# Optimization experiments

Measured on AMD Instinct MI355X. Metric: run time of the kernel, lower is better.

## Reference

```python
import jax, jax.numpy as jnp
import numpy as np

N = 100_000      # nodes
E = 3_200_000    # edges (avg degree 32)
H = 16           # hidden channels
C_IN, C_OUT = 1, 2


def setup_inputs() -> dict:
    key = jax.random.key(0)
    k1, k2, k3, k4, k5 = jax.random.split(key, 5)
    x = jax.random.normal(k1, (N, C_IN), dtype=jnp.float32)
    src = jax.random.randint(k2, (E,), 0, N, dtype=jnp.int32)
    dst = jax.random.randint(k3, (E,), 0, N, dtype=jnp.int32)
    edge_index = jnp.stack([src, dst])  # [2, E], PyG layout
    # Glorot-style init for the two linear transforms
    W1 = jax.random.normal(k4, (C_IN, H), dtype=jnp.float32) * np.sqrt(2.0 / (C_IN + H))
    b1 = jnp.zeros((H,), dtype=jnp.float32)
    W2 = jax.random.normal(k5, (H, C_OUT), dtype=jnp.float32) * np.sqrt(2.0 / (H + C_OUT))
    b2 = jnp.zeros((C_OUT,), dtype=jnp.float32)
    return {"x": x, "edge_index": edge_index, "W1": W1, "b1": b1, "W2": W2, "b2": b2}


def _gcn_conv(x, src, dst, W, b):
    """GCNConv: out = D^{-1/2} (A+I) D^{-1/2} X W + b.
    src/dst already include self-loops. x: [N, Cin], W: [Cin, Cout]."""
    deg = jax.ops.segment_sum(jnp.ones_like(dst, dtype=x.dtype), dst, num_segments=N)
    dinv = jnp.where(deg > 0, jax.lax.rsqrt(jnp.maximum(deg, 1.0)), 0.0)
    norm = dinv[src] * dinv[dst]                       # [E+N]
    h = x @ W                                          # transform first (Cin small)
    msg = norm[:, None] * h[src]                       # [E+N, Cout]
    out = jax.ops.segment_sum(msg, dst, num_segments=N)
    return out + b


def reference(x, edge_index, W1, b1, W2, b2):
    loops = jnp.arange(N, dtype=edge_index.dtype)
    src = jnp.concatenate([edge_index[0], loops])      # add self-loops
    dst = jnp.concatenate([edge_index[1], loops])
    h = _gcn_conv(x, src, dst, W1, b1)
    h = jax.nn.relu(h)
    out = _gcn_conv(h, src, dst, W2, b2)
    return out
```

## Files before the change

kernel.cpp:

```cpp
#include <hip/hip_runtime.h>

#define NN 100000
#define NE 3200000
#define HC 16

#define BKT_BITS 7
#define BKT_NODES 128
#define NB 782
#define NB1 783
#define CHUNK_S 8192
#define NCH 391
#define NCCP 392
#define MCAP 5120
#define PADW (((unsigned)NN << BKT_BITS) | (BKT_NODES - 1))

typedef unsigned uv4 __attribute__((ext_vector_type(4)));
typedef int      iv4 __attribute__((ext_vector_type(4)));


__global__ __launch_bounds__(512) void k_sortchunk(const int* __restrict__ src,
                                                   const int* __restrict__ dst,
                                                   unsigned short* __restrict__ Hoff,
                                                   unsigned* __restrict__ binned) {
    __shared__ unsigned h[NB1];
    __shared__ unsigned sorted[CHUNK_S];
    __shared__ unsigned wsum[8];
    int tid = threadIdx.x;
    int c = blockIdx.x;
    int b0 = c * CHUNK_S;
    int e1 = min(b0 + CHUNK_S, NE);
    int cnt = e1 - b0;

    for (int j = tid; j < NB1; j += 512) h[j] = 0;
    __syncthreads();

    iv4 dreg[4], sreg[4];
    int nit = 0;
    for (int v = b0 + tid * 4; v + 3 < e1; v += 2048) {
        iv4 d4 = *(const iv4*)(dst + v);
        iv4 s4 = *(const iv4*)(src + v);
        dreg[nit] = d4; sreg[nit] = s4; ++nit;
        atomicAdd(&h[((unsigned)d4.x) >> BKT_BITS], 1u);
        atomicAdd(&h[((unsigned)d4.y) >> BKT_BITS], 1u);
        atomicAdd(&h[((unsigned)d4.z) >> BKT_BITS], 1u);
        atomicAdd(&h[((unsigned)d4.w) >> BKT_BITS], 1u);
    }
    __syncthreads();

    int i0 = tid * 2;
    unsigned v0 = (i0 + 0 < NB1) ? h[i0 + 0] : 0;
    unsigned v1 = (i0 + 1 < NB1) ? h[i0 + 1] : 0;
    unsigned lsum = v0 + v1;
    unsigned sc = lsum;
#pragma unroll
    for (int off = 1; off < 64; off <<= 1) {
        unsigned u = __shfl_up(sc, off, 64);
        if ((tid & 63) >= off) sc += u;
    }
    int wave = tid >> 6;
    if ((tid & 63) == 63) wsum[wave] = sc;
    __syncthreads();
    unsigned wpre = 0;
    for (int w = 0; w < wave; ++w) wpre += wsum[w];
    unsigned excl = wpre + sc - lsum;
    __syncthreads();
    if (i0 + 0 < NB1) h[i0 + 0] = excl;
    if (i0 + 1 < NB1) h[i0 + 1] = excl + v0;

    unsigned short* row = Hoff + (size_t)c * NB1;
    if (i0 + 0 < NB1) row[i0 + 0] = (unsigned short)excl;
    if (i0 + 1 < NB1) row[i0 + 1] = (unsigned short)(excl + v0);
    __syncthreads();

    int it = 0;
    for (int v = b0 + tid * 4; v + 3 < e1; v += 2048, ++it) {
        iv4 d4 = dreg[it];
        iv4 s4 = sreg[it];
        {   unsigned d = (unsigned)d4.x, s = (unsigned)s4.x;
            unsigned pos = atomicAdd(&h[d >> BKT_BITS], 1u);
            sorted[pos] = (s << BKT_BITS) | (d & (BKT_NODES - 1)); }
        {   unsigned d = (unsigned)d4.y, s = (unsigned)s4.y;
            unsigned pos = atomicAdd(&h[d >> BKT_BITS], 1u);
            sorted[pos] = (s << BKT_BITS) | (d & (BKT_NODES - 1)); }
        {   unsigned d = (unsigned)d4.z, s = (unsigned)s4.z;
            unsigned pos = atomicAdd(&h[d >> BKT_BITS], 1u);
            sorted[pos] = (s << BKT_BITS) | (d & (BKT_NODES - 1)); }
        {   unsigned d = (unsigned)d4.w, s = (unsigned)s4.w;
            unsigned pos = atomicAdd(&h[d >> BKT_BITS], 1u);
            sorted[pos] = (s << BKT_BITS) | (d & (BKT_NODES - 1)); }
    }
    __syncthreads();

    unsigned* out = binned + (size_t)c * CHUNK_S;
    for (int j = tid * 4; j + 3 < cnt; j += 2048)
        *(uv4*)(out + j) = *(const uv4*)(sorted + j);
}


__global__ __launch_bounds__(256) void k_transT(const unsigned short* __restrict__ Hoff,
                                                unsigned short* __restrict__ TH) {
    __shared__ unsigned short tile[32][33];
    int tx = threadIdx.x & 31;
    int ty0 = (threadIdx.x >> 5) * 4;
    int c0 = blockIdx.x * 32;
    int b0 = blockIdx.y * 32;
#pragma unroll
    for (int k = 0; k < 4; ++k) {
        int c = c0 + ty0 + k, b = b0 + tx;
        tile[ty0 + k][tx] = (c < NCH && b < NB1) ? Hoff[(size_t)c * NB1 + b] : (unsigned short)0;
    }
    __syncthreads();
#pragma unroll
    for (int k = 0; k < 4; ++k) {
        int b = b0 + ty0 + k, c = c0 + tx;
        if (b < NB1 && c < NCH) TH[(size_t)b * NCCP + c] = tile[tx][ty0 + k];
    }
}


__global__ __launch_bounds__(64) void k_totals(const unsigned short* __restrict__ TH,
                                               unsigned* __restrict__ totals) {
    int b = blockIdx.x;
    int lane = threadIdx.x;
    const unsigned short* r0 = TH + (size_t)b * NCCP;
    const unsigned short* r1 = r0 + NCCP;
    unsigned s = 0;
    for (int c = lane; c < NCH; c += 64) s += (unsigned)r1[c] - (unsigned)r0[c];
#pragma unroll
    for (int off = 32; off >= 1; off >>= 1) s += __shfl_xor(s, off, 64);
    if (lane == 0) totals[b] = s;
}

__global__ __launch_bounds__(1024) void k_base2(const unsigned* __restrict__ totals,
                                                unsigned* __restrict__ gbase) {
    __shared__ unsigned s[1024];
    int t = threadIdx.x;
    unsigned v = (t < NB) ? ((totals[t] + 15u) & ~15u) : 0;
    s[t] = v;
    __syncthreads();
    for (int off = 1; off < 1024; off <<= 1) {
        unsigned u = (t >= off) ? s[t - off] : 0;
        __syncthreads();
        s[t] += u;
        __syncthreads();
    }
    if (t < NB) gbase[t] = s[t] - v;
}


__global__ __launch_bounds__(256) void k_merge_deg(const unsigned* __restrict__ binned,
                                                   const unsigned short* __restrict__ TH,
                                                   const unsigned* __restrict__ gbase,
                                                   const float* __restrict__ x,
                                                   unsigned* __restrict__ merged,
                                                   unsigned short* __restrict__ cofsg,
                                                   float* __restrict__ dinv,
                                                   float* __restrict__ p) {
    __shared__ unsigned short th0s[NCH];
    __shared__ unsigned short lens[NCH];
    __shared__ unsigned S[NCH + 1];
    __shared__ unsigned wsum[4];
    __shared__ unsigned cnt[BKT_NODES];
    __shared__ unsigned stage[MCAP];
    __shared__ unsigned short cof[BKT_NODES + 2];
    __shared__ unsigned wsA;
    int tid = threadIdx.x, b = blockIdx.x;

    const unsigned short* r0 = TH + (size_t)b * NCCP;
    const unsigned short* r1 = r0 + NCCP;
    for (int c = tid; c < NCH; c += 256) {
        unsigned a = r0[c];
        th0s[c] = (unsigned short)a;
        lens[c] = (unsigned short)((unsigned)r1[c] - a);
    }
    if (tid < BKT_NODES) cnt[tid] = 0;
    __syncthreads();

    int i0 = tid * 2;
    unsigned v0 = (i0 + 0 < NCH) ? (unsigned)lens[i0 + 0] : 0;
    unsigned v1 = (i0 + 1 < NCH) ? (unsigned)lens[i0 + 1] : 0;
    unsigned lsum = v0 + v1;
    unsigned sc = lsum;
#pragma unroll
    for (int off = 1; off < 64; off <<= 1) {
        unsigned u = __shfl_up(sc, off, 64);
        if ((tid & 63) >= off) sc += u;
    }
    int wave = tid >> 6;
    if ((tid & 63) == 63) wsum[wave] = sc;
    __syncthreads();
    unsigned wpre = 0;
    for (int w = 0; w < wave; ++w) wpre += wsum[w];
    unsigned excl = wpre + sc - lsum;
    if (i0 + 0 <= NCH) S[i0 + 0] = excl;
    if (i0 + 1 <= NCH) S[i0 + 1] = excl + v0;
    __syncthreads();

    unsigned T = S[NCH];
    unsigned Tr = (T + 15u) & ~15u;
    unsigned gb = gbase[b];
    if (tid < 16) {
        unsigned q = T + tid;
        if (q < Tr) stage[q] = PADW;
    }

    for (int c = tid; c < NCH; c += 256) {
        unsigned off = th0s[c], L = lens[c];
        if (!L) continue;
        unsigned base = S[c];
        const unsigned* segbase = binned + (size_t)c * CHUNK_S;
        unsigned je = off + L;
        for (unsigned j4 = off & ~3u; j4 < je; j4 += 4) {
            uv4 e4 = *(const uv4*)(segbase + j4);
#pragma unroll
            for (int k = 0; k < 4; ++k) {
                unsigned j = j4 + (unsigned)k;
                if (j >= off && j < je) {
                    unsigned e = ((const unsigned*)&e4)[k];
                    atomicAdd(&cnt[e & (BKT_NODES - 1)], 1u);
                    stage[base + (j - off)] = e;
                }
            }
        }
    }
    __syncthreads();

    for (unsigned j = tid * 4; j < Tr; j += 1024)
        *(uv4*)(merged + gb + j) = *(const uv4*)(stage + j);

    unsigned cv = (tid < BKT_NODES) ? cnt[tid] : 0u;
    unsigned csc = cv;
#pragma unroll
    for (int off = 1; off < 64; off <<= 1) {
        unsigned u = __shfl_up(csc, off, 64);
        if ((tid & 63) >= off) csc += u;
    }
    if (tid == 63) wsA = csc;
    __syncthreads();
    if (tid < BKT_NODES) {
        unsigned incl = csc + ((tid >= 64) ? wsA : 0u);
        cof[tid + 1] = (unsigned short)incl;
    }
    if (tid == 0) cof[0] = 0;
    __syncthreads();
    if (tid < BKT_NODES + 1)
        cofsg[(size_t)b * (BKT_NODES + 2) + tid] = cof[tid];

    int node = b * BKT_NODES + tid;
    if (tid < BKT_NODES) {
        if (node < NN) {
            float di = rsqrtf((float)(cnt[tid] + 1u));
            dinv[node] = di;
            p[node] = di * x[node];
        } else if (node == NN) {
            p[node] = 0.f;
        }
    }
}


__global__ __launch_bounds__(512) void k_agg1(unsigned* __restrict__ merged,
                                              const unsigned* __restrict__ gbase,
                                              const unsigned* __restrict__ totals,
                                              const unsigned short* __restrict__ cofsg,
                                              const float* __restrict__ dinv,
                                              const float* __restrict__ p,
                                              const float* __restrict__ W1,
                                              const float* __restrict__ b1,
                                              const float* __restrict__ W2,
                                              float2* __restrict__ g) {
    __shared__ unsigned short cof[BKT_NODES + 2];
    __shared__ unsigned cur[BKT_NODES + 1];
    __shared__ unsigned se[MCAP];
    __shared__ float part[512];
    int tid = threadIdx.x, b = blockIdx.x;
    if (tid < BKT_NODES + 1) cof[tid] = cofsg[(size_t)b * (BKT_NODES + 2) + tid];
    __syncthreads();
    if (tid < BKT_NODES + 1) cur[tid] = cof[tid];
    __syncthreads();
    unsigned Tr = (totals[b] + 15u) & ~15u;
    unsigned* m = merged + gbase[b];
    for (unsigned j = tid * 4; j < Tr; j += 2048) {
        uv4 e = *(const uv4*)(m + j);
        { unsigned w = e.x; unsigned sl = (w >> BKT_BITS >= NN) ? 128u : (w & (BKT_NODES - 1));
          se[atomicAdd(&cur[sl], 1u)] = w >> BKT_BITS; }
        { unsigned w = e.y; unsigned sl = (w >> BKT_BITS >= NN) ? 128u : (w & (BKT_NODES - 1));
          se[atomicAdd(&cur[sl], 1u)] = w >> BKT_BITS; }
        { unsigned w = e.z; unsigned sl = (w >> BKT_BITS >= NN) ? 128u : (w & (BKT_NODES - 1));
          se[atomicAdd(&cur[sl], 1u)] = w >> BKT_BITS; }
        { unsigned w = e.w; unsigned sl = (w >> BKT_BITS >= NN) ? 128u : (w & (BKT_NODES - 1));
          se[atomicAdd(&cur[sl], 1u)] = w >> BKT_BITS; }
    }
    __syncthreads();

    for (unsigned j = tid * 4; j < Tr; j += 2048)
        *(uv4*)(m + j) = *(const uv4*)(se + j);

    int nl = tid >> 2, q = tid & 3;
    unsigned o0 = cof[nl], o1 = cof[nl + 1];
    unsigned len = o1 - o0;
    unsigned s = o0 + ((len * q) >> 2);
    unsigned e = o0 + ((len * (q + 1)) >> 2);
    float sum = 0.f;
    unsigned i = s;
    for (; i + 3 < e; i += 4) {
        unsigned a0 = se[i], a1 = se[i + 1], a2 = se[i + 2], a3 = se[i + 3];
        float x0 = p[a0], x1 = p[a1], x2 = p[a2], x3 = p[a3];
        sum += (x0 + x1) + (x2 + x3);
    }
    for (; i < e; ++i) sum += p[se[i]];
    part[tid] = sum;
    __syncthreads();

    if (q == 0) {
        int node = b * BKT_NODES + nl;
        if (node < NN) {
            float di = dinv[node];
            float sf = di * (part[tid] + part[tid + 1] + part[tid + 2] + part[tid + 3]
                             + p[node]);
            float g0 = 0.f, g1 = 0.f;
#pragma unroll
            for (int c = 0; c < HC; ++c) {
                float h = fmaxf(fmaf(sf, W1[c], b1[c]), 0.f);
                g0 = fmaf(h, W2[2 * c], g0);
                g1 = fmaf(h, W2[2 * c + 1], g1);
            }
            g[node] = make_float2(di * g0, di * g1);
        }
    }
}


__global__ __launch_bounds__(512) void k_agg2(const unsigned* __restrict__ merged,
                                              const unsigned* __restrict__ gbase,
                                              const unsigned* __restrict__ totals,
                                              const unsigned short* __restrict__ cofsg,
                                              const float* __restrict__ dinv,
                                              const float2* __restrict__ g,
                                              const float* __restrict__ b2,
                                              float2* __restrict__ out) {
    __shared__ unsigned short cof[BKT_NODES + 2];
    __shared__ unsigned se[MCAP];
    __shared__ float2 part[512];
    int tid = threadIdx.x, b = blockIdx.x;
    if (tid < BKT_NODES + 1) cof[tid] = cofsg[(size_t)b * (BKT_NODES + 2) + tid];
    unsigned Tr = (totals[b] + 15u) & ~15u;
    const unsigned* m = merged + gbase[b];
    for (unsigned j = tid * 4; j < Tr; j += 2048)
        *(uv4*)(se + j) = *(const uv4*)(m + j);
    __syncthreads();

    int nl = tid >> 2, q = tid & 3;
    unsigned o0 = cof[nl], o1 = cof[nl + 1];
    unsigned len = o1 - o0;
    unsigned s = o0 + ((len * q) >> 2);
    unsigned e = o0 + ((len * (q + 1)) >> 2);
    float sx = 0.f, sy = 0.f;
    unsigned i = s;
    for (; i + 3 < e; i += 4) {
        unsigned a0 = se[i], a1 = se[i + 1], a2 = se[i + 2], a3 = se[i + 3];
        float2 v0 = g[a0], v1 = g[a1], v2 = g[a2], v3 = g[a3];
        sx += (v0.x + v1.x) + (v2.x + v3.x);
        sy += (v0.y + v1.y) + (v2.y + v3.y);
    }
    for (; i < e; ++i) { float2 v = g[se[i]]; sx += v.x; sy += v.y; }
    part[tid] = make_float2(sx, sy);
    __syncthreads();

    if (q == 0) {
        int node = b * BKT_NODES + nl;
        if (node < NN) {
            float di = dinv[node];
            float2 me = g[node];
            float ax = part[tid].x + part[tid + 1].x + part[tid + 2].x + part[tid + 3].x + me.x;
            float ay = part[tid].y + part[tid + 1].y + part[tid + 2].y + part[tid + 3].y + me.y;
            out[node] = make_float2(fmaf(di, ax, b2[0]), fmaf(di, ay, b2[1]));
        }
    }
}


__global__ __launch_bounds__(256) void f_deg(const int* __restrict__ dst,
                                             unsigned int* __restrict__ deg, int E) {
    int i = blockIdx.x * blockDim.x + threadIdx.x;
    if (i < E) atomicAdd(&deg[dst[i]], 1u);
}
__global__ __launch_bounds__(256) void f_node1(const float* __restrict__ x,
                                               const unsigned int* __restrict__ deg,
                                               float* __restrict__ dinv, float* __restrict__ p,
                                               float* __restrict__ t, int N) {
    int i = blockIdx.x * blockDim.x + threadIdx.x;
    if (i < N) {
        float di = rsqrtf((float)(deg[i] + 1u));
        dinv[i] = di; float pi = di * x[i]; p[i] = pi; t[i] = pi;
    }
}
__global__ __launch_bounds__(256) void f_scatter1(const int* __restrict__ src,
                                                  const int* __restrict__ dst,
                                                  const float* __restrict__ p,
                                                  float* __restrict__ t, int E) {
    int i = blockIdx.x * blockDim.x + threadIdx.x;
    if (i < E) atomicAdd(&t[dst[i]], p[src[i]]);
}
__global__ __launch_bounds__(256) void f_node2(const float* __restrict__ dinv,
                                               const float* __restrict__ t,
                                               const float* __restrict__ W1,
                                               const float* __restrict__ b1,
                                               const float* __restrict__ W2,
                                               float2* __restrict__ g,
                                               float2* __restrict__ acc, int N) {
    int i = blockIdx.x * blockDim.x + threadIdx.x;
    if (i < N) {
        float di = dinv[i]; float s = di * t[i];
        float g0 = 0.f, g1 = 0.f;
#pragma unroll
        for (int c = 0; c < HC; ++c) {
            float h = fmaxf(fmaf(s, W1[c], b1[c]), 0.f);
            g0 = fmaf(h, W2[2 * c], g0); g1 = fmaf(h, W2[2 * c + 1], g1);
        }
        float2 gv = make_float2(di * g0, di * g1);
        g[i] = gv; acc[i] = gv;
    }
}
__global__ __launch_bounds__(256) void f_scatter2(const int* __restrict__ src,
                                                  const int* __restrict__ dst,
                                                  const float2* __restrict__ g,
                                                  float* __restrict__ acc, int E) {
    int i = blockIdx.x * blockDim.x + threadIdx.x;
    if (i < E) {
        int s = src[i], d = dst[i];
        float2 gv = g[s];
        atomicAdd(&acc[2 * d], gv.x);
        atomicAdd(&acc[2 * d + 1], gv.y);
    }
}
__global__ __launch_bounds__(256) void f_out(const float* __restrict__ dinv,
                                             const float* __restrict__ b2,
                                             float* __restrict__ out, int N) {
    int i = blockIdx.x * blockDim.x + threadIdx.x;
    if (i < N) {
        float di = dinv[i];
        out[2 * i]     = fmaf(di, out[2 * i],     b2[0]);
        out[2 * i + 1] = fmaf(di, out[2 * i + 1], b2[1]);
    }
}

extern "C" void kernel_launch(void* const* d_in, const int* in_sizes, int n_in,
                              void* d_out, int out_size, void* d_ws, size_t ws_size,
                              hipStream_t stream) {
    const float* x  = (const float*)d_in[0];
    const int* ei   = (const int*)d_in[1];
    const int* src  = ei;
    const int* dst  = ei + NE;
    const float* W1 = (const float*)d_in[2];
    const float* b1 = (const float*)d_in[3];
    const float* W2 = (const float*)d_in[4];
    const float* b2 = (const float*)d_in[5];

    const int BT = 256;
    const int gridE = (NE + BT - 1) / BT;
    const int gridN = (NN + BT - 1) / BT;

    size_t need = 0;
    auto carve = [&](size_t bytes) { size_t o = need; need += (bytes + 255) & ~(size_t)255; return o; };
    size_t o_Hoff = carve((size_t)NCH * NB1 * 2);
    size_t o_TH   = carve((size_t)NB1 * NCCP * 2);
    size_t o_tot  = carve((size_t)NB * 4);
    size_t o_gb   = carve((size_t)(NB + 1) * 4);
    size_t o_cofs = carve((size_t)NB * (BKT_NODES + 2) * 2);
    size_t o_dinv = carve((size_t)NN * 4);
    size_t o_p    = carve((size_t)(NN + 1) * 4);
    size_t o_g    = carve((size_t)(NN + 1) * 8);
    size_t o_bin  = carve((size_t)NCH * CHUNK_S * 4);
    size_t o_mrg  = carve((size_t)(NE + 16 * NB + 64) * 4);

    if (ws_size >= need) {
        char* ws = (char*)d_ws;
        unsigned short* Hoff = (unsigned short*)(ws + o_Hoff);
        unsigned short* TH   = (unsigned short*)(ws + o_TH);
        unsigned* totals = (unsigned*)(ws + o_tot);
        unsigned* gbase  = (unsigned*)(ws + o_gb);
        unsigned short* cofs = (unsigned short*)(ws + o_cofs);
        float*    dinv   = (float*)(ws + o_dinv);
        float*    p      = (float*)(ws + o_p);
        float2*   g      = (float2*)(ws + o_g);
        unsigned* binned = (unsigned*)(ws + o_bin);
        unsigned* merged = (unsigned*)(ws + o_mrg);

        k_sortchunk<<<NCH, 512, 0, stream>>>(src, dst, Hoff, binned);
        k_transT   <<<dim3(13, 25), 256, 0, stream>>>(Hoff, TH);
        k_totals   <<<NB, 64, 0, stream>>>(TH, totals);
        k_base2    <<<1, 1024, 0, stream>>>(totals, gbase);
        k_merge_deg<<<NB, 256, 0, stream>>>(binned, TH, gbase, x, merged, cofs, dinv, p);
        k_agg1     <<<NB, 512, 0, stream>>>(merged, gbase, totals, cofs, dinv, p, W1, b1, W2, g);
        k_agg2     <<<NB, 512, 0, stream>>>(merged, gbase, totals, cofs, dinv, g, b2, (float2*)d_out);
    } else {
        float* out = (float*)d_out;
        char* ws = (char*)d_ws;
        unsigned int* deg = (unsigned int*)ws;
        float* dinv = (float*)(ws + 1 * sizeof(float) * NN);
        float* p    = (float*)(ws + 2 * sizeof(float) * NN);
        float* t    = (float*)(ws + 3 * sizeof(float) * NN);
        float2* g   = (float2*)(ws + 4 * sizeof(float) * NN);

        hipMemsetAsync(deg, 0, NN * sizeof(unsigned int), stream);
        f_deg<<<gridE, BT, 0, stream>>>(dst, deg, NE);
        f_node1<<<gridN, BT, 0, stream>>>(x, deg, dinv, p, t, NN);
        f_scatter1<<<gridE, BT, 0, stream>>>(src, dst, p, t, NE);
        f_node2<<<gridN, BT, 0, stream>>>(dinv, t, W1, b1, W2, g, (float2*)out, NN);
        f_scatter2<<<gridE, BT, 0, stream>>>(src, dst, g, out, NE);
        f_out<<<gridN, BT, 0, stream>>>(dinv, b2, out, NN);
    }
}
```

Before: 148.8 us.

## Replace chunk sort/merge pipeline with atomic-reserved fixed-capacity bucket regions

```diff
diff --git a/kernel.cpp b/kernel.cpp
--- a/kernel.cpp
+++ b/kernel.cpp
@@ -7,31 +7,25 @@
 #define BKT_BITS 7
 #define BKT_NODES 128
 #define NB 782
-#define NB1 783
 #define CHUNK_S 8192
 #define NCH 391
-#define NCCP 392
 #define MCAP 5120
-#define PADW (((unsigned)NN << BKT_BITS) | (BKT_NODES - 1))
 
 typedef unsigned uv4 __attribute__((ext_vector_type(4)));
 typedef int      iv4 __attribute__((ext_vector_type(4)));
 
 
-__global__ __launch_bounds__(512) void k_sortchunk(const int* __restrict__ src,
-                                                   const int* __restrict__ dst,
-                                                   unsigned short* __restrict__ Hoff,
-                                                   unsigned* __restrict__ binned) {
-    __shared__ unsigned h[NB1];
-    __shared__ unsigned sorted[CHUNK_S];
-    __shared__ unsigned wsum[8];
+__global__ __launch_bounds__(512) void k_bin(const int* __restrict__ src,
+                                             const int* __restrict__ dst,
+                                             unsigned* __restrict__ gcur,
+                                             unsigned* __restrict__ regions) {
+    __shared__ unsigned h[NB];
     int tid = threadIdx.x;
     int c = blockIdx.x;
     int b0 = c * CHUNK_S;
     int e1 = min(b0 + CHUNK_S, NE);
-    int cnt = e1 - b0;
-
-    for (int j = tid; j < NB1; j += 512) h[j] = 0;
+
+    for (int j = tid; j < NB; j += 512) h[j] = 0;
     __syncthreads();
 
     iv4 dreg[4], sreg[4];
@@ -47,29 +41,10 @@
     }
     __syncthreads();
 
-    int i0 = tid * 2;
-    unsigned v0 = (i0 + 0 < NB1) ? h[i0 + 0] : 0;
-    unsigned v1 = (i0 + 1 < NB1) ? h[i0 + 1] : 0;
-    unsigned lsum = v0 + v1;
-    unsigned sc = lsum;
-#pragma unroll
-    for (int off = 1; off < 64; off <<= 1) {
-        unsigned u = __shfl_up(sc, off, 64);
-        if ((tid & 63) >= off) sc += u;
-    }
-    int wave = tid >> 6;
-    if ((tid & 63) == 63) wsum[wave] = sc;
-    __syncthreads();
-    unsigned wpre = 0;
-    for (int w = 0; w < wave; ++w) wpre += wsum[w];
-    unsigned excl = wpre + sc - lsum;
-    __syncthreads();
-    if (i0 + 0 < NB1) h[i0 + 0] = excl;
-    if (i0 + 1 < NB1) h[i0 + 1] = excl + v0;
-
-    unsigned short* row = Hoff + (size_t)c * NB1;
-    if (i0 + 0 < NB1) row[i0 + 0] = (unsigned short)excl;
-    if (i0 + 1 < NB1) row[i0 + 1] = (unsigned short)(excl + v0);
+    for (int j = tid; j < NB; j += 512) {
+        unsigned cEdges = h[j];
+        if (cEdges) h[j] = (unsigned)j * MCAP + atomicAdd(&gcur[j], cEdges);
+    }
     __syncthreads();
 
     int it = 0;
@@ -78,246 +53,93 @@
         iv4 s4 = sreg[it];
         {   unsigned d = (unsigned)d4.x, s = (unsigned)s4.x;
             unsigned pos = atomicAdd(&h[d >> BKT_BITS], 1u);
-            sorted[pos] = (s << BKT_BITS) | (d & (BKT_NODES - 1)); }
+            regions[pos] = (s << BKT_BITS) | (d & (BKT_NODES - 1)); }
         {   unsigned d = (unsigned)d4.y, s = (unsigned)s4.y;
             unsigned pos = atomicAdd(&h[d >> BKT_BITS], 1u);
-            sorted[pos] = (s << BKT_BITS) | (d & (BKT_NODES - 1)); }
+            regions[pos] = (s << BKT_BITS) | (d & (BKT_NODES - 1)); }
         {   unsigned d = (unsigned)d4.z, s = (unsigned)s4.z;
             unsigned pos = atomicAdd(&h[d >> BKT_BITS], 1u);
-            sorted[pos] = (s << BKT_BITS) | (d & (BKT_NODES - 1)); }
+            regions[pos] = (s << BKT_BITS) | (d & (BKT_NODES - 1)); }
         {   unsigned d = (unsigned)d4.w, s = (unsigned)s4.w;
             unsigned pos = atomicAdd(&h[d >> BKT_BITS], 1u);
-            sorted[pos] = (s << BKT_BITS) | (d & (BKT_NODES - 1)); }
-    }
-    __syncthreads();
-
-    unsigned* out = binned + (size_t)c * CHUNK_S;
-    for (int j = tid * 4; j + 3 < cnt; j += 2048)
-        *(uv4*)(out + j) = *(const uv4*)(sorted + j);
-}
-
-
-__global__ __launch_bounds__(256) void k_transT(const unsigned short* __restrict__ Hoff,
-                                                unsigned short* __restrict__ TH) {
-    __shared__ unsigned short tile[32][33];
-    int tx = threadIdx.x & 31;
-    int ty0 = (threadIdx.x >> 5) * 4;
-    int c0 = blockIdx.x * 32;
-    int b0 = blockIdx.y * 32;
-#pragma unroll
-    for (int k = 0; k < 4; ++k) {
-        int c = c0 + ty0 + k, b = b0 + tx;
-        tile[ty0 + k][tx] = (c < NCH && b < NB1) ? Hoff[(size_t)c * NB1 + b] : (unsigned short)0;
-    }
-    __syncthreads();
-#pragma unroll
-    for (int k = 0; k < 4; ++k) {
-        int b = b0 + ty0 + k, c = c0 + tx;
-        if (b < NB1 && c < NCH) TH[(size_t)b * NCCP + c] = tile[tx][ty0 + k];
-    }
-}
-
-
-__global__ __launch_bounds__(64) void k_totals(const unsigned short* __restrict__ TH,
-                                               unsigned* __restrict__ totals) {
-    int b = blockIdx.x;
-    int lane = threadIdx.x;
-    const unsigned short* r0 = TH + (size_t)b * NCCP;
-    const unsigned short* r1 = r0 + NCCP;
-    unsigned s = 0;
-    for (int c = lane; c < NCH; c += 64) s += (unsigned)r1[c] - (unsigned)r0[c];
-#pragma unroll
-    for (int off = 32; off >= 1; off >>= 1) s += __shfl_xor(s, off, 64);
-    if (lane == 0) totals[b] = s;
-}
-
-__global__ __launch_bounds__(1024) void k_base2(const unsigned* __restrict__ totals,
-                                                unsigned* __restrict__ gbase) {
-    __shared__ unsigned s[1024];
-    int t = threadIdx.x;
-    unsigned v = (t < NB) ? ((totals[t] + 15u) & ~15u) : 0;
-    s[t] = v;
-    __syncthreads();
-    for (int off = 1; off < 1024; off <<= 1) {
-        unsigned u = (t >= off) ? s[t - off] : 0;
-        __syncthreads();
-        s[t] += u;
-        __syncthreads();
-    }
-    if (t < NB) gbase[t] = s[t] - v;
-}
-
-
-__global__ __launch_bounds__(256) void k_merge_deg(const unsigned* __restrict__ binned,
-                                                   const unsigned short* __restrict__ TH,
-                                                   const unsigned* __restrict__ gbase,
-                                                   const float* __restrict__ x,
-                                                   unsigned* __restrict__ merged,
-                                                   unsigned short* __restrict__ cofsg,
-                                                   float* __restrict__ dinv,
-                                                   float* __restrict__ p) {
-    __shared__ unsigned short th0s[NCH];
-    __shared__ unsigned short lens[NCH];
-    __shared__ unsigned S[NCH + 1];
-    __shared__ unsigned wsum[4];
+            regions[pos] = (s << BKT_BITS) | (d & (BKT_NODES - 1)); }
+    }
+}
+
+
+__global__ __launch_bounds__(256) void k_deg(const unsigned* __restrict__ regions,
+                                             const unsigned* __restrict__ gcur,
+                                             const float* __restrict__ x,
+                                             float* __restrict__ dinv,
+                                             float* __restrict__ p) {
     __shared__ unsigned cnt[BKT_NODES];
-    __shared__ unsigned stage[MCAP];
-    __shared__ unsigned short cof[BKT_NODES + 2];
-    __shared__ unsigned wsA;
     int tid = threadIdx.x, b = blockIdx.x;
-
-    const unsigned short* r0 = TH + (size_t)b * NCCP;
-    const unsigned short* r1 = r0 + NCCP;
-    for (int c = tid; c < NCH; c += 256) {
-        unsigned a = r0[c];
-        th0s[c] = (unsigned short)a;
-        lens[c] = (unsigned short)((unsigned)r1[c] - a);
-    }
     if (tid < BKT_NODES) cnt[tid] = 0;
     __syncthreads();
 
-    int i0 = tid * 2;
-    unsigned v0 = (i0 + 0 < NCH) ? (unsigned)lens[i0 + 0] : 0;
-    unsigned v1 = (i0 + 1 < NCH) ? (unsigned)lens[i0 + 1] : 0;
-    unsigned lsum = v0 + v1;
-    unsigned sc = lsum;
-#pragma unroll
-    for (int off = 1; off < 64; off <<= 1) {
-        unsigned u = __shfl_up(sc, off, 64);
-        if ((tid & 63) >= off) sc += u;
-    }
-    int wave = tid >> 6;
-    if ((tid & 63) == 63) wsum[wave] = sc;
-    __syncthreads();
-    unsigned wpre = 0;
-    for (int w = 0; w < wave; ++w) wpre += wsum[w];
-    unsigned excl = wpre + sc - lsum;
-    if (i0 + 0 <= NCH) S[i0 + 0] = excl;
-    if (i0 + 1 <= NCH) S[i0 + 1] = excl + v0;
-    __syncthreads();
-
-    unsigned T = S[NCH];
-    unsigned Tr = (T + 15u) & ~15u;
-    unsigned gb = gbase[b];
-    if (tid < 16) {
-        unsigned q = T + tid;
-        if (q < Tr) stage[q] = PADW;
-    }
-
-    for (int c = tid; c < NCH; c += 256) {
-        unsigned off = th0s[c], L = lens[c];
-        if (!L) continue;
-        unsigned base = S[c];
-        const unsigned* segbase = binned + (size_t)c * CHUNK_S;
-        unsigned je = off + L;
-        for (unsigned j4 = off & ~3u; j4 < je; j4 += 4) {
-            uv4 e4 = *(const uv4*)(segbase + j4);
-#pragma unroll
-            for (int k = 0; k < 4; ++k) {
-                unsigned j = j4 + (unsigned)k;
-                if (j >= off && j < je) {
-                    unsigned e = ((const unsigned*)&e4)[k];
-                    atomicAdd(&cnt[e & (BKT_NODES - 1)], 1u);
-                    stage[base + (j - off)] = e;
-                }
-            }
-        }
-    }
-    __syncthreads();
-
-    for (unsigned j = tid * 4; j < Tr; j += 1024)
-        *(uv4*)(merged + gb + j) = *(const uv4*)(stage + j);
-
-    unsigned cv = (tid < BKT_NODES) ? cnt[tid] : 0u;
-    unsigned csc = cv;
-#pragma unroll
-    for (int off = 1; off < 64; off <<= 1) {
-        unsigned u = __shfl_up(csc, off, 64);
-        if ((tid & 63) >= off) csc += u;
-    }
-    if (tid == 63) wsA = csc;
-    __syncthreads();
+    unsigned sz = gcur[b];
+    const unsigned* r = regions + (size_t)b * MCAP;
+    unsigned sz4 = sz & ~3u;
+    for (unsigned j = (unsigned)tid * 4; j < sz4; j += 1024) {
+        uv4 e = *(const uv4*)(r + j);
+        atomicAdd(&cnt[e.x & (BKT_NODES - 1)], 1u);
+        atomicAdd(&cnt[e.y & (BKT_NODES - 1)], 1u);
+        atomicAdd(&cnt[e.z & (BKT_NODES - 1)], 1u);
+        atomicAdd(&cnt[e.w & (BKT_NODES - 1)], 1u);
+    }
+    for (unsigned j = sz4 + (unsigned)tid; j < sz; j += 256)
+        atomicAdd(&cnt[r[j] & (BKT_NODES - 1)], 1u);
+    __syncthreads();
+
     if (tid < BKT_NODES) {
-        unsigned incl = csc + ((tid >= 64) ? wsA : 0u);
-        cof[tid + 1] = (unsigned short)incl;
-    }
-    if (tid == 0) cof[0] = 0;
-    __syncthreads();
-    if (tid < BKT_NODES + 1)
-        cofsg[(size_t)b * (BKT_NODES + 2) + tid] = cof[tid];
-
-    int node = b * BKT_NODES + tid;
-    if (tid < BKT_NODES) {
+        int node = b * BKT_NODES + tid;
         if (node < NN) {
             float di = rsqrtf((float)(cnt[tid] + 1u));
             dinv[node] = di;
             p[node] = di * x[node];
-        } else if (node == NN) {
-            p[node] = 0.f;
         }
     }
 }
 
 
-__global__ __launch_bounds__(512) void k_agg1(unsigned* __restrict__ merged,
-                                              const unsigned* __restrict__ gbase,
-                                              const unsigned* __restrict__ totals,
-                                              const unsigned short* __restrict__ cofsg,
+__global__ __launch_bounds__(256) void k_agg1(const unsigned* __restrict__ regions,
+                                              const unsigned* __restrict__ gcur,
                                               const float* __restrict__ dinv,
                                               const float* __restrict__ p,
                                               const float* __restrict__ W1,
                                               const float* __restrict__ b1,
                                               const float* __restrict__ W2,
                                               float2* __restrict__ g) {
-    __shared__ unsigned short cof[BKT_NODES + 2];
-    __shared__ unsigned cur[BKT_NODES + 1];
-    __shared__ unsigned se[MCAP];
-    __shared__ float part[512];
+    __shared__ float acc[BKT_NODES];
     int tid = threadIdx.x, b = blockIdx.x;
-    if (tid < BKT_NODES + 1) cof[tid] = cofsg[(size_t)b * (BKT_NODES + 2) + tid];
-    __syncthreads();
-    if (tid < BKT_NODES + 1) cur[tid] = cof[tid];
-    __syncthreads();
-    unsigned Tr = (totals[b] + 15u) & ~15u;
-    unsigned* m = merged + gbase[b];
-    for (unsigned j = tid * 4; j < Tr; j += 2048) {
-        uv4 e = *(const uv4*)(m + j);
-        { unsigned w = e.x; unsigned sl = (w >> BKT_BITS >= NN) ? 128u : (w & (BKT_NODES - 1));
-          se[atomicAdd(&cur[sl], 1u)] = w >> BKT_BITS; }
-        { unsigned w = e.y; unsigned sl = (w >> BKT_BITS >= NN) ? 128u : (w & (BKT_NODES - 1));
-          se[atomicAdd(&cur[sl], 1u)] = w >> BKT_BITS; }
-        { unsigned w = e.z; unsigned sl = (w >> BKT_BITS >= NN) ? 128u : (w & (BKT_NODES - 1));
-          se[atomicAdd(&cur[sl], 1u)] = w >> BKT_BITS; }
-        { unsigned w = e.w; unsigned sl = (w >> BKT_BITS >= NN) ? 128u : (w & (BKT_NODES - 1));
-          se[atomicAdd(&cur[sl], 1u)] = w >> BKT_BITS; }
-    }
-    __syncthreads();
-
-    for (unsigned j = tid * 4; j < Tr; j += 2048)
-        *(uv4*)(m + j) = *(const uv4*)(se + j);
-
-    int nl = tid >> 2, q = tid & 3;
-    unsigned o0 = cof[nl], o1 = cof[nl + 1];
-    unsigned len = o1 - o0;
-    unsigned s = o0 + ((len * q) >> 2);
-    unsigned e = o0 + ((len * (q + 1)) >> 2);
-    float sum = 0.f;
-    unsigned i = s;
-    for (; i + 3 < e; i += 4) {
-        unsigned a0 = se[i], a1 = se[i + 1], a2 = se[i + 2], a3 = se[i + 3];
-        float x0 = p[a0], x1 = p[a1], x2 = p[a2], x3 = p[a3];
-        sum += (x0 + x1) + (x2 + x3);
-    }
-    for (; i < e; ++i) sum += p[se[i]];
-    part[tid] = sum;
-    __syncthreads();
-
-    if (q == 0) {
-        int node = b * BKT_NODES + nl;
+    if (tid < BKT_NODES) acc[tid] = 0.f;
+    __syncthreads();
+
+    unsigned sz = gcur[b];
+    const unsigned* r = regions + (size_t)b * MCAP;
+    unsigned sz4 = sz & ~3u;
+    for (unsigned j = (unsigned)tid * 4; j < sz4; j += 1024) {
+        uv4 e = *(const uv4*)(r + j);
+        float p0 = p[e.x >> BKT_BITS];
+        float p1 = p[e.y >> BKT_BITS];
+        float p2 = p[e.z >> BKT_BITS];
+        float p3 = p[e.w >> BKT_BITS];
+        atomicAdd(&acc[e.x & (BKT_NODES - 1)], p0);
+        atomicAdd(&acc[e.y & (BKT_NODES - 1)], p1);
+        atomicAdd(&acc[e.z & (BKT_NODES - 1)], p2);
+        atomicAdd(&acc[e.w & (BKT_NODES - 1)], p3);
+    }
+    for (unsigned j = sz4 + (unsigned)tid; j < sz; j += 256) {
+        unsigned e = r[j];
+        atomicAdd(&acc[e & (BKT_NODES - 1)], p[e >> BKT_BITS]);
+    }
+    __syncthreads();
+
+    if (tid < BKT_NODES) {
+        int node = b * BKT_NODES + tid;
         if (node < NN) {
             float di = dinv[node];
-            float sf = di * (part[tid] + part[tid + 1] + part[tid + 2] + part[tid + 3]
-                             + p[node]);
+            float sf = di * (acc[tid] + p[node]);
             float g0 = 0.f, g1 = 0.f;
 #pragma unroll
             for (int c = 0; c < HC; ++c) {
@@ -331,49 +153,51 @@
 }
 
 
-__global__ __launch_bounds__(512) void k_agg2(const unsigned* __restrict__ merged,
-                                              const unsigned* __restrict__ gbase,
-                                              const unsigned* __restrict__ totals,
-                                              const unsigned short* __restrict__ cofsg,
+__global__ __launch_bounds__(256) void k_agg2(const unsigned* __restrict__ regions,
+                                              const unsigned* __restrict__ gcur,
                                               const float* __restrict__ dinv,
                                               const float2* __restrict__ g,
                                               const float* __restrict__ b2,
                                               float2* __restrict__ out) {
-    __shared__ unsigned short cof[BKT_NODES + 2];
-    __shared__ unsigned se[MCAP];
-    __shared__ float2 part[512];
+    __shared__ float accx[BKT_NODES];
+    __shared__ float accy[BKT_NODES];
     int tid = threadIdx.x, b = blockIdx.x;
-    if (tid < BKT_NODES + 1) cof[tid] = cofsg[(size_t)b * (BKT_NODES + 2) + tid];
-    unsigned Tr = (totals[b] + 15u) & ~15u;
-    const unsigned* m = merged + gbase[b];
-    for (unsigned j = tid * 4; j < Tr; j += 2048)
-        *(uv4*)(se + j) = *(const uv4*)(m + j);
-    __syncthreads();
-
-    int nl = tid >> 2, q = tid & 3;
-    unsigned o0 = cof[nl], o1 = cof[nl + 1];
-    unsigned len = o1 - o0;
-    unsigned s = o0 + ((len * q) >> 2);
-    unsigned e = o0 + ((len * (q + 1)) >> 2);
-    float sx = 0.f, sy = 0.f;
-    unsigned i = s;
-    for (; i + 3 < e; i += 4) {
-        unsigned a0 = se[i], a1 = se[i + 1], a2 = se[i + 2], a3 = se[i + 3];
-        float2 v0 = g[a0], v1 = g[a1], v2 = g[a2], v3 = g[a3];
-        sx += (v0.x + v1.x) + (v2.x + v3.x);
-        sy += (v0.y + v1.y) + (v2.y + v3.y);
-    }
-    for (; i < e; ++i) { float2 v = g[se[i]]; sx += v.x; sy += v.y; }
-    part[tid] = make_float2(sx, sy);
-    __syncthreads();
-
-    if (q == 0) {
-        int node = b * BKT_NODES + nl;
+    if (tid < BKT_NODES) { accx[tid] = 0.f; accy[tid] = 0.f; }
+    __syncthreads();
+
+    unsigned sz = gcur[b];
+    const unsigned* r = regions + (size_t)b * MCAP;
+    unsigned sz4 = sz & ~3u;
+    for (unsigned j = (unsigned)tid * 4; j < sz4; j += 1024) {
+        uv4 e = *(const uv4*)(r + j);
+        float2 v0 = g[e.x >> BKT_BITS];
+        float2 v1 = g[e.y >> BKT_BITS];
+        float2 v2 = g[e.z >> BKT_BITS];
+        float2 v3 = g[e.w >> BKT_BITS];
+        atomicAdd(&accx[e.x & (BKT_NODES - 1)], v0.x);
+        atomicAdd(&accy[e.x & (BKT_NODES - 1)], v0.y);
+        atomicAdd(&accx[e.y & (BKT_NODES - 1)], v1.x);
+        atomicAdd(&accy[e.y & (BKT_NODES - 1)], v1.y);
+        atomicAdd(&accx[e.z & (BKT_NODES - 1)], v2.x);
+        atomicAdd(&accy[e.z & (BKT_NODES - 1)], v2.y);
+        atomicAdd(&accx[e.w & (BKT_NODES - 1)], v3.x);
+        atomicAdd(&accy[e.w & (BKT_NODES - 1)], v3.y);
+    }
+    for (unsigned j = sz4 + (unsigned)tid; j < sz; j += 256) {
+        unsigned e = r[j];
+        float2 v = g[e >> BKT_BITS];
+        atomicAdd(&accx[e & (BKT_NODES - 1)], v.x);
+        atomicAdd(&accy[e & (BKT_NODES - 1)], v.y);
+    }
+    __syncthreads();
+
+    if (tid < BKT_NODES) {
+        int node = b * BKT_NODES + tid;
         if (node < NN) {
             float di = dinv[node];
             float2 me = g[node];
-            float ax = part[tid].x + part[tid + 1].x + part[tid + 2].x + part[tid + 3].x + me.x;
-            float ay = part[tid].y + part[tid + 1].y + part[tid + 2].y + part[tid + 3].y + me.y;
+            float ax = accx[tid] + me.x;
+            float ay = accy[tid] + me.y;
             out[node] = make_float2(fmaf(di, ax, b2[0]), fmaf(di, ay, b2[1]));
         }
     }
@@ -463,37 +287,25 @@
 
     size_t need = 0;
     auto carve = [&](size_t bytes) { size_t o = need; need += (bytes + 255) & ~(size_t)255; return o; };
-    size_t o_Hoff = carve((size_t)NCH * NB1 * 2);
-    size_t o_TH   = carve((size_t)NB1 * NCCP * 2);
-    size_t o_tot  = carve((size_t)NB * 4);
-    size_t o_gb   = carve((size_t)(NB + 1) * 4);
-    size_t o_cofs = carve((size_t)NB * (BKT_NODES + 2) * 2);
+    size_t o_gcur = carve((size_t)NB * 4);
     size_t o_dinv = carve((size_t)NN * 4);
-    size_t o_p    = carve((size_t)(NN + 1) * 4);
-    size_t o_g    = carve((size_t)(NN + 1) * 8);
-    size_t o_bin  = carve((size_t)NCH * CHUNK_S * 4);
-    size_t o_mrg  = carve((size_t)(NE + 16 * NB + 64) * 4);
+    size_t o_p    = carve((size_t)NN * 4);
+    size_t o_g    = carve((size_t)NN * 8);
+    size_t o_reg  = carve((size_t)NB * MCAP * 4);
 
     if (ws_size >= need) {
         char* ws = (char*)d_ws;
-        unsigned short* Hoff = (unsigned short*)(ws + o_Hoff);
-        unsigned short* TH   = (unsigned short*)(ws + o_TH);
-        unsigned* totals = (unsigned*)(ws + o_tot);
-        unsigned* gbase  = (unsigned*)(ws + o_gb);
-        unsigned short* cofs = (unsigned short*)(ws + o_cofs);
+        unsigned* gcur   = (unsigned*)(ws + o_gcur);
         float*    dinv   = (float*)(ws + o_dinv);
         float*    p      = (float*)(ws + o_p);
         float2*   g      = (float2*)(ws + o_g);
-        unsigned* binned = (unsigned*)(ws + o_bin);
-        unsigned* merged = (unsigned*)(ws + o_mrg);
-
-        k_sortchunk<<<NCH, 512, 0, stream>>>(src, dst, Hoff, binned);
-        k_transT   <<<dim3(13, 25), 256, 0, stream>>>(Hoff, TH);
-        k_totals   <<<NB, 64, 0, stream>>>(TH, totals);
-        k_base2    <<<1, 1024, 0, stream>>>(totals, gbase);
-        k_merge_deg<<<NB, 256, 0, stream>>>(binned, TH, gbase, x, merged, cofs, dinv, p);
-        k_agg1     <<<NB, 512, 0, stream>>>(merged, gbase, totals, cofs, dinv, p, W1, b1, W2, g);
-        k_agg2     <<<NB, 512, 0, stream>>>(merged, gbase, totals, cofs, dinv, g, b2, (float2*)d_out);
+        unsigned* regions= (unsigned*)(ws + o_reg);
+
+        hipMemsetAsync(gcur, 0, (size_t)NB * 4, stream);
+        k_bin <<<NCH, 512, 0, stream>>>(src, dst, gcur, regions);
+        k_deg <<<NB, 256, 0, stream>>>(regions, gcur, x, dinv, p);
+        k_agg1<<<NB, 256, 0, stream>>>(regions, gcur, dinv, p, W1, b1, W2, g);
+        k_agg2<<<NB, 256, 0, stream>>>(regions, gcur, dinv, g, b2, (float2*)d_out);
     } else {
         float* out = (float*)d_out;
         char* ws = (char*)d_ws;
```

Result: slower. 179.6 us (+20.7%).
